# Kernel optimization log

Measured on AMD Instinct MI355X. Metric: run time of the kernel, lower is better.

Reference implementation:

```python
import jax, jax.numpy as jnp
import numpy as np

N_NODES = 8192
IN_F = 16384
OUT_F = 10
N_EDGES = 262144


def setup_inputs() -> dict:
    key = jax.random.key(0)
    ks = jax.random.split(key, 12)
    s = 0.02
    return {
        "x": jax.random.normal(ks[0], (N_NODES, IN_F), dtype=jnp.float32),
        "edge_index": jax.random.randint(ks[1], (2, N_EDGES), 0, N_NODES, dtype=jnp.int64),
        # lin1: in -> 4096, lin2: 4096 -> 2048 (torch Linear: y = x W^T + b)
        "lin1_w": jax.random.normal(ks[2], (4096, IN_F), dtype=jnp.float32) * s,
        "lin1_b": jnp.zeros((4096,), dtype=jnp.float32),
        "lin2_w": jax.random.normal(ks[3], (2048, 4096), dtype=jnp.float32) * s,
        "lin2_b": jnp.zeros((2048,), dtype=jnp.float32),
        # SAGEConv 1: 2048 -> 1024. lin_l (neighbor agg, with bias), lin_r (root, no bias)
        "s1_l_w": jax.random.normal(ks[4], (1024, 2048), dtype=jnp.float32) * s,
        "s1_l_b": jnp.zeros((1024,), dtype=jnp.float32),
        "s1_r_w": jax.random.normal(ks[5], (1024, 2048), dtype=jnp.float32) * s,
        # SAGEConv 2: 1024 -> OUT_F
        "s2_l_w": jax.random.normal(ks[6], (OUT_F, 1024), dtype=jnp.float32) * s,
        "s2_l_b": jnp.zeros((OUT_F,), dtype=jnp.float32),
        "s2_r_w": jax.random.normal(ks[7], (OUT_F, 1024), dtype=jnp.float32) * s,
    }


def reference(x, edge_index, lin1_w, lin1_b, lin2_w, lin2_b,
              s1_l_w, s1_l_b, s1_r_w, s2_l_w, s2_l_b, s2_r_w):
    n = x.shape[0]
    src, dst = edge_index[0], edge_index[1]
    # in-degree for mean aggregation; isolated nodes -> 0 aggregate (PyG behavior)
    deg = jax.ops.segment_sum(jnp.ones_like(dst, dtype=x.dtype), dst, num_segments=n)
    inv_deg = jnp.where(deg > 0, 1.0 / jnp.maximum(deg, 1.0), 0.0)[:, None]

    def sage(h, lw, lb, rw):
        # mean over incoming neighbor messages h[src] scattered to dst
        agg = jax.ops.segment_sum(h[src], dst, num_segments=n) * inv_deg
        return agg @ lw.T + lb + h @ rw.T

    h = jax.nn.relu(x @ lin1_w.T + lin1_b)
    h = jax.nn.relu(h @ lin2_w.T + lin2_b)
    # dropout layers act as identity in eval mode
    h = jax.nn.relu(sage(h, s1_l_w, s1_l_b, s1_r_w))
    h = jax.nn.relu(sage(h, s2_l_w, s2_l_b, s2_r_w))
    return jax.nn.softmax(h, axis=1)
```

## Files before the change

kernel.cpp:

```cpp
#include <hip/hip_runtime.h>


typedef short  short8   __attribute__((ext_vector_type(8)));
typedef float  floatx4  __attribute__((ext_vector_type(4)));
typedef unsigned short ushort8v __attribute__((ext_vector_type(8)));
typedef unsigned short ushort4v __attribute__((ext_vector_type(4)));
typedef unsigned short ushort;

__device__ __forceinline__ ushort f2bf(float f) {
  unsigned u = __float_as_uint(f);
  u += 0x7fffu + ((u >> 16) & 1u);
  return (ushort)(u >> 16);
}
__device__ __forceinline__ float bf2f(ushort h) {
  return __uint_as_float(((unsigned)h) << 16);
}

__device__ __forceinline__ void gload16(const void* g, void* l) {
  __builtin_amdgcn_global_load_lds(
      (const __attribute__((address_space(1))) void*)g,
      (__attribute__((address_space(3))) void*)l, 16, 0, 0);
}

__global__ __launch_bounds__(256) void cvt_f32_bf16(
    const float* __restrict__ in, ushort* __restrict__ out, long n8) {
  long i = (long)blockIdx.x * blockDim.x + threadIdx.x;
  const long stride = (long)gridDim.x * blockDim.x;
  for (; i < n8; i += stride) {
    const float4* p = (const float4*)(in + i * 8);
    float4 a = p[0], b = p[1];
    ushort8v o;
    o[0] = f2bf(a.x); o[1] = f2bf(a.y); o[2] = f2bf(a.z); o[3] = f2bf(a.w);
    o[4] = f2bf(b.x); o[5] = f2bf(b.y); o[6] = f2bf(b.z); o[7] = f2bf(b.w);
    *(ushort8v*)(out + i * 8) = o;
  }
}

__global__ void edge_count(const int* __restrict__ dst, int E, int* __restrict__ deg) {
  int e = blockIdx.x * 256 + threadIdx.x;
  if (e < E) atomicAdd(&deg[dst[e]], 1);
}

__global__ __launch_bounds__(256) void scan_k(
    const int* __restrict__ deg, int* __restrict__ offs, float* __restrict__ inv, int n) {
  __shared__ int part[256];
  const int t = threadIdx.x;
  int local[32];
  int s = 0;
  const int base = t * 32;
#pragma unroll
  for (int i = 0; i < 32; ++i) { local[i] = s; s += deg[base + i]; }
  part[t] = s;
  __syncthreads();
  for (int off = 1; off < 256; off <<= 1) {
    int v = (t >= off) ? part[t - off] : 0;
    __syncthreads();
    part[t] += v;
    __syncthreads();
  }
  const int prev = (t == 0) ? 0 : part[t - 1];
  if (t == 255) offs[n] = part[255];
#pragma unroll
  for (int i = 0; i < 32; ++i) {
    const int e = base + i;
    offs[e] = prev + local[i];
    const int d = deg[e];
    inv[e] = (d > 0) ? (1.0f / (float)d) : 0.0f;
  }
}

__global__ void edge_fill(const int* __restrict__ src, const int* __restrict__ dst, int E,
                          const int* __restrict__ offs, int* __restrict__ fill,
                          int* __restrict__ csr) {
  int e = blockIdx.x * 256 + threadIdx.x;
  if (e < E) {
    const int d = dst[e];
    const int p = offs[d] + atomicAdd(&fill[d], 1);
    csr[p] = src[e];
  }
}

template <int OUT_BF16, int RELU, int HAS_BIAS>
__global__ __launch_bounds__(512, 2) void gemm256(
    const ushort* __restrict__ A, const ushort* __restrict__ Bm,
    const float* __restrict__ bias, void* __restrict__ Cout,
    int M, int N, int K) {
  extern __shared__ char smem[];

  const int nbn = N >> 8;
  const int nbm8 = (M >> 8) >> 3;
  const int x = blockIdx.x & 7;
  const int j = blockIdx.x >> 3;
  const int bm = x * nbm8 + j / nbn;
  const int bn = j % nbn;

  const int t = threadIdx.x;
  const int w = t >> 6, lane = t & 63;
  const int wr = w >> 2, wc = w & 3;

  const int cswz = (t & 7) ^ ((t >> 3) & 7);
  const ushort* Ag = A  + (size_t)(bm * 256 + (t >> 3)) * K + cswz * 8;
  const ushort* Bg = Bm + (size_t)(bn * 256 + (t >> 3)) * K + cswz * 8;
  const int stOff = w * 1024;

  const int rA = wr * 128 + (lane & 15);
  const int rB = wc * 64 + (lane & 15);
  const int s0 = (((lane >> 4) ^ (lane & 7)) << 4);

  floatx4 acc[8][4] = {};
  const int NT = K >> 6;

  {
    char* la = smem + stOff;
    char* lb = la + 32768;
#pragma unroll
    for (int i = 0; i < 4; ++i) gload16(Ag + (size_t)(i * 64) * K, la + i * 8192);
#pragma unroll
    for (int i = 0; i < 4; ++i) gload16(Bg + (size_t)(i * 64) * K, lb + i * 8192);
  }
  __syncthreads();

  for (int kt = 0; kt < NT; ++kt) {
    const char* pa = smem + (kt & 1) * 65536 + rA * 128;
    const char* pb = smem + (kt & 1) * 65536 + 32768 + rB * 128;

    short8 a0[8], b0[4];
#pragma unroll
    for (int mi = 0; mi < 8; ++mi) a0[mi] = *(const short8*)(pa + mi * 2048 + s0);
#pragma unroll
    for (int ni = 0; ni < 4; ++ni) b0[ni] = *(const short8*)(pb + ni * 2048 + s0);

    if (kt + 1 < NT) {
      const int k0 = (kt + 1) << 6;
      char* la = smem + ((kt + 1) & 1) * 65536 + stOff;
      char* lb = la + 32768;
#pragma unroll
      for (int i = 0; i < 4; ++i) gload16(Ag + (size_t)(i * 64) * K + k0, la + i * 8192);
#pragma unroll
      for (int i = 0; i < 4; ++i) gload16(Bg + (size_t)(i * 64) * K + k0, lb + i * 8192);
    }

#pragma unroll
    for (int mi = 0; mi < 8; ++mi)
#pragma unroll
      for (int ni = 0; ni < 4; ++ni)
        acc[mi][ni] = __builtin_amdgcn_mfma_f32_16x16x32_bf16(a0[mi], b0[ni], acc[mi][ni], 0, 0, 0);

    short8 a1[8], b1[4];
#pragma unroll
    for (int mi = 0; mi < 8; ++mi) a1[mi] = *(const short8*)(pa + mi * 2048 + (s0 ^ 64));
#pragma unroll
    for (int ni = 0; ni < 4; ++ni) b1[ni] = *(const short8*)(pb + ni * 2048 + (s0 ^ 64));

#pragma unroll
    for (int mi = 0; mi < 8; ++mi)
#pragma unroll
      for (int ni = 0; ni < 4; ++ni)
        acc[mi][ni] = __builtin_amdgcn_mfma_f32_16x16x32_bf16(a1[mi], b1[ni], acc[mi][ni], 0, 0, 0);

    __syncthreads();
  }

  const int row0 = bm * 256 + wr * 128 + ((lane >> 4) << 2);
  const int col0 = bn * 256 + wc * 64 + (lane & 15);
#pragma unroll
  for (int ni = 0; ni < 4; ++ni) {
    const int col = col0 + ni * 16;
    const float bv = HAS_BIAS ? bias[col] : 0.0f;
#pragma unroll
    for (int mi = 0; mi < 8; ++mi) {
#pragma unroll
      for (int j2 = 0; j2 < 4; ++j2) {
        const int row = row0 + mi * 16 + j2;
        float v = acc[mi][ni][j2] + bv;
        if (RELU) v = fmaxf(v, 0.0f);
        if (OUT_BF16)
          ((ushort*)Cout)[(size_t)row * N + col] = f2bf(v);
        else
          ((float*)Cout)[(size_t)row * N + col] = v;
      }
    }
  }
}

__global__ __launch_bounds__(256) void sage1_agg(
    const ushort* __restrict__ hlr1, const int* __restrict__ offs,
    const int* __restrict__ csr, const float* __restrict__ inv,
    const float* __restrict__ lb, ushort* __restrict__ h3) {
  const int dn = blockIdx.x;
  const int f4 = threadIdx.x * 4;
  float ax = 0.f, ay = 0.f, az = 0.f, aw = 0.f;
  const int e0 = offs[dn], e1 = offs[dn + 1];
  for (int e = e0; e < e1; ++e) {
    const int s = csr[e];
    const ushort4v v = *(const ushort4v*)(hlr1 + (size_t)s * 2048 + f4);
    ax += bf2f(v[0]); ay += bf2f(v[1]); az += bf2f(v[2]); aw += bf2f(v[3]);
  }
  const float iv = inv[dn];
  const ushort4v hr = *(const ushort4v*)(hlr1 + (size_t)dn * 2048 + 1024 + f4);
  const float4 bb = *(const float4*)(lb + f4);
  ushort4v o;
  o[0] = f2bf(fmaxf(ax * iv + bb.x + bf2f(hr[0]), 0.0f));
  o[1] = f2bf(fmaxf(ay * iv + bb.y + bf2f(hr[1]), 0.0f));
  o[2] = f2bf(fmaxf(az * iv + bb.z + bf2f(hr[2]), 0.0f));
  o[3] = f2bf(fmaxf(aw * iv + bb.w + bf2f(hr[3]), 0.0f));
  *(ushort4v*)(h3 + (size_t)dn * 1024 + f4) = o;
}

__global__ __launch_bounds__(256) void sage2_mm(
    const ushort* __restrict__ h3, const float* __restrict__ wl,
    const float* __restrict__ wr, float* __restrict__ hl2, float* __restrict__ hr2) {
  __shared__ float wds[20480];
  const int t = threadIdx.x;
  for (int i = t; i < 2560; i += 256)
    *(float4*)&wds[i * 4] = *(const float4*)&wl[i * 4];
  for (int i = t; i < 2560; i += 256)
    *(float4*)&wds[10240 + i * 4] = *(const float4*)&wr[i * 4];
  __syncthreads();

  const int r = t >> 4, c = t & 15;
  const int row = blockIdx.x * 16 + r;

  float hv[64];
#pragma unroll
  for (int ii = 0; ii < 8; ++ii) {
    ushort8v p = *(const ushort8v*)(h3 + (size_t)row * 1024 + c * 64 + ii * 8);
#pragma unroll
    for (int k = 0; k < 8; ++k) hv[ii * 8 + k] = bf2f(p[k]);
  }

  float al[10] = {}, ar[10] = {};
#pragma unroll
  for (int j = 0; j < 10; ++j) {
    const int base = j * 1024 + c * 64;
#pragma unroll
    for (int ii = 0; ii < 16; ++ii) {
      const int f = (ii + c) & 15;
      const float4 lv = *(const float4*)&wds[base + f * 4];
      const float4 rv = *(const float4*)&wds[10240 + base + f * 4];
      const float h0 = hv[f * 4], h1 = hv[f * 4 + 1],
                  h2 = hv[f * 4 + 2], h3v = hv[f * 4 + 3];
      al[j] = fmaf(h0, lv.x, fmaf(h1, lv.y, fmaf(h2, lv.z, fmaf(h3v, lv.w, al[j]))));
      ar[j] = fmaf(h0, rv.x, fmaf(h1, rv.y, fmaf(h2, rv.z, fmaf(h3v, rv.w, ar[j]))));
    }
  }
#pragma unroll
  for (int j = 0; j < 10; ++j) {
#pragma unroll
    for (int off = 8; off > 0; off >>= 1) {
      al[j] += __shfl_down(al[j], off);
      ar[j] += __shfl_down(ar[j], off);
    }
  }
  if (c == 0) {
#pragma unroll
    for (int j = 0; j < 10; ++j) {
      hl2[(size_t)row * 10 + j] = al[j];
      hr2[(size_t)row * 10 + j] = ar[j];
    }
  }
}

__global__ __launch_bounds__(64) void sage2_final(
    const float* __restrict__ hl2, const float* __restrict__ hr2,
    const int* __restrict__ offs, const int* __restrict__ csr,
    const float* __restrict__ inv, const float* __restrict__ lb,
    float* __restrict__ out) {
  const int dn = blockIdx.x;
  const int l = threadIdx.x;
  float a[10] = {};
  const int e0 = offs[dn], e1 = offs[dn + 1];
  for (int e = e0 + l; e < e1; e += 64) {
    const int s = csr[e];
#pragma unroll
    for (int j = 0; j < 10; ++j) a[j] += hl2[(size_t)s * 10 + j];
  }
#pragma unroll
  for (int j = 0; j < 10; ++j)
#pragma unroll
    for (int off = 32; off > 0; off >>= 1) a[j] += __shfl_down(a[j], off);
  if (l == 0) {
    const float iv = inv[dn];
    float v[10];
    float m = -1e30f;
#pragma unroll
    for (int j = 0; j < 10; ++j) {
      v[j] = fmaxf(a[j] * iv + lb[j] + hr2[(size_t)dn * 10 + j], 0.0f);
      m = fmaxf(m, v[j]);
    }
    float ssum = 0.0f;
#pragma unroll
    for (int j = 0; j < 10; ++j) { v[j] = __expf(v[j] - m); ssum += v[j]; }
    const float r = 1.0f / ssum;
#pragma unroll
    for (int j = 0; j < 10; ++j) out[(size_t)dn * 10 + j] = v[j] * r;
  }
}

extern "C" void kernel_launch(void* const* d_in, const int* in_sizes, int n_in,
                              void* d_out, int out_size, void* d_ws, size_t ws_size,
                              hipStream_t stream) {
  const float* x    = (const float*)d_in[0];
  const int*   ei   = (const int*)d_in[1];
  const float* w1   = (const float*)d_in[2];
  const float* b1   = (const float*)d_in[3];
  const float* w2   = (const float*)d_in[4];
  const float* b2   = (const float*)d_in[5];
  const float* s1lw = (const float*)d_in[6];
  const float* s1lb = (const float*)d_in[7];
  const float* s1rw = (const float*)d_in[8];
  const float* s2lw = (const float*)d_in[9];
  const float* s2lb = (const float*)d_in[10];
  const float* s2rw = (const float*)d_in[11];
  float* out = (float*)d_out;
  char* ws = (char*)d_ws;

  const int E = in_sizes[1] / 2;
  const int Nn = 8192;

  hipFuncSetAttribute((const void*)&gemm256<1, 1, 1>,
                      hipFuncAttributeMaxDynamicSharedMemorySize, 131072);
  hipFuncSetAttribute((const void*)&gemm256<1, 0, 0>,
                      hipFuncAttributeMaxDynamicSharedMemorySize, 131072);

  ushort* xb  = (ushort*)(ws + 0L);
  ushort* w1b = (ushort*)(ws + 268435456L);
  ushort* h1  = (ushort*)(ws + 402653184L);
  ushort* w2b = (ushort*)(ws + 469762048L);
  ushort* h2  = (ushort*)(ws + 486539264L);
  ushort* ws1 = (ushort*)(ws + 520093696L);
  char* csrb = ws + 528482304L;
  int*   deg  = (int*)(csrb);
  int*   fill = (int*)(csrb + 32768);
  int*   offs = (int*)(csrb + 65536);
  float* inv  = (float*)(csrb + 98816);
  int*   csr  = (int*)(csrb + 131584);
  ushort* hlr1 = (ushort*)(ws + 0L);
  ushort* h3   = (ushort*)(ws + 67108864L);
  float*  hl2  = (float*)(ws + 83886080L);
  float*  hr2  = (float*)(ws + 84213760L);

  const int* esrc = ei;
  const int* edst = ei + E;

  hipMemsetAsync(deg, 0, 65536, stream);

  cvt_f32_bf16<<<4096, 256, 0, stream>>>(x, xb, 16777216L);
  cvt_f32_bf16<<<2048, 256, 0, stream>>>(w1, w1b, 8388608L);
  cvt_f32_bf16<<<1024, 256, 0, stream>>>(w2, w2b, 1048576L);
  cvt_f32_bf16<<<256, 256, 0, stream>>>(s1lw, ws1, 262144L);
  cvt_f32_bf16<<<256, 256, 0, stream>>>(s1rw, ws1 + 2097152L, 262144L);

  edge_count<<<(E + 255) / 256, 256, 0, stream>>>(edst, E, deg);
  scan_k<<<1, 256, 0, stream>>>(deg, offs, inv, Nn);
  edge_fill<<<(E + 255) / 256, 256, 0, stream>>>(esrc, edst, E, offs, fill, csr);

  gemm256<1, 1, 1><<<512, 512, 131072, stream>>>(xb, w1b, b1, h1, 8192, 4096, 16384);
  gemm256<1, 1, 1><<<256, 512, 131072, stream>>>(h1, w2b, b2, h2, 8192, 2048, 4096);
  gemm256<1, 0, 0><<<256, 512, 131072, stream>>>(h2, ws1, nullptr, hlr1, 8192, 2048, 2048);

  sage1_agg<<<8192, 256, 0, stream>>>(hlr1, offs, csr, inv, s1lb, h3);
  sage2_mm<<<512, 256, 0, stream>>>(h3, s2lw, s2rw, hl2, hr2);
  sage2_final<<<8192, 64, 0, stream>>>(hl2, hr2, offs, csr, inv, s2lb, out);
}
```

Before: 1.673 ms.

## Restructure GEMM main loop into fine-grained phases with interleaved async loads

Replaces the simple double-buffered k-loop with an 8-phase schedule per two k-tiles. Each phase reads a slice of A fragments, issues a portion of the next tile's global-to-LDS loads, waits with explicit vmcnt counts, and raises wave priority around the MFMA bursts. The goal is to hide global load latency and LDS reads behind MFMA work instead of stalling at a full __syncthreads each tile. It relies on hand-tuned waitcnt values and per-phase barriers, assumes NT is even, and issues dummy loads past the last tile.

```diff
diff --git a/kernel.cpp b/kernel.cpp
--- a/kernel.cpp
+++ b/kernel.cpp
@@ -109,57 +109,83 @@
 
   floatx4 acc[8][4] = {};
   const int NT = K >> 6;
-
-  {
-    char* la = smem + stOff;
-    char* lb = la + 32768;
-#pragma unroll
-    for (int i = 0; i < 4; ++i) gload16(Ag + (size_t)(i * 64) * K, la + i * 8192);
-#pragma unroll
-    for (int i = 0; i < 4; ++i) gload16(Bg + (size_t)(i * 64) * K, lb + i * 8192);
-  }
-  __syncthreads();
-
-  for (int kt = 0; kt < NT; ++kt) {
-    const char* pa = smem + (kt & 1) * 65536 + rA * 128;
-    const char* pb = smem + (kt & 1) * 65536 + 32768 + rB * 128;
-
-    short8 a0[8], b0[4];
-#pragma unroll
-    for (int mi = 0; mi < 8; ++mi) a0[mi] = *(const short8*)(pa + mi * 2048 + s0);
-#pragma unroll
-    for (int ni = 0; ni < 4; ++ni) b0[ni] = *(const short8*)(pb + ni * 2048 + s0);
-
-    if (kt + 1 < NT) {
-      const int k0 = (kt + 1) << 6;
-      char* la = smem + ((kt + 1) & 1) * 65536 + stOff;
-      char* lb = la + 32768;
-#pragma unroll
-      for (int i = 0; i < 4; ++i) gload16(Ag + (size_t)(i * 64) * K + k0, la + i * 8192);
-#pragma unroll
-      for (int i = 0; i < 4; ++i) gload16(Bg + (size_t)(i * 64) * K + k0, lb + i * 8192);
-    }
-
-#pragma unroll
-    for (int mi = 0; mi < 8; ++mi)
-#pragma unroll
-      for (int ni = 0; ni < 4; ++ni)
-        acc[mi][ni] = __builtin_amdgcn_mfma_f32_16x16x32_bf16(a0[mi], b0[ni], acc[mi][ni], 0, 0, 0);
-
-    short8 a1[8], b1[4];
-#pragma unroll
-    for (int mi = 0; mi < 8; ++mi) a1[mi] = *(const short8*)(pa + mi * 2048 + (s0 ^ 64));
-#pragma unroll
-    for (int ni = 0; ni < 4; ++ni) b1[ni] = *(const short8*)(pb + ni * 2048 + (s0 ^ 64));
-
-#pragma unroll
-    for (int mi = 0; mi < 8; ++mi)
-#pragma unroll
-      for (int ni = 0; ni < 4; ++ni)
-        acc[mi][ni] = __builtin_amdgcn_mfma_f32_16x16x32_bf16(a1[mi], b1[ni], acc[mi][ni], 0, 0, 0);
-
-    __syncthreads();
-  }
+  const int NIT = NT >> 1;
+
+#define STGA(BUF, KT, H)                                                      \
+  {                                                                           \
+    const int k0_ = (((KT) < NT) ? (KT) : 0) << 6;                            \
+    char* la_ = smem + (BUF) * 65536 + stOff;                                 \
+    gload16(Ag + (size_t)(((H) * 2) * 64) * K + k0_, la_ + ((H) * 2) * 8192); \
+    gload16(Ag + (size_t)(((H) * 2 + 1) * 64) * K + k0_,                      \
+            la_ + ((H) * 2 + 1) * 8192);                                      \
+  }
+#define STGB(BUF, KT, H)                                                      \
+  {                                                                           \
+    const int k0_ = (((KT) < NT) ? (KT) : 0) << 6;                            \
+    char* lb_ = smem + (BUF) * 65536 + 32768 + stOff;                         \
+    gload16(Bg + (size_t)(((H) * 2) * 64) * K + k0_, lb_ + ((H) * 2) * 8192); \
+    gload16(Bg + (size_t)(((H) * 2 + 1) * 64) * K + k0_,                      \
+            lb_ + ((H) * 2 + 1) * 8192);                                      \
+  }
+
+#define PH(BUF, Q, READB, DOWAIT, ...)                                        \
+  {                                                                           \
+    const char* pa_ = smem + (BUF) * 65536 + rA * 128;                        \
+    short8 a00 = *(const short8*)(pa_ + (2 * (Q)) * 2048 + s0);               \
+    short8 a01 = *(const short8*)(pa_ + (2 * (Q)) * 2048 + (s0 ^ 64));        \
+    short8 a10 = *(const short8*)(pa_ + (2 * (Q) + 1) * 2048 + s0);           \
+    short8 a11 = *(const short8*)(pa_ + (2 * (Q) + 1) * 2048 + (s0 ^ 64));    \
+    if (READB) {                                                              \
+      const char* pb_ = smem + (BUF) * 65536 + 32768 + rB * 128;              \
+      _Pragma("unroll") for (int ni = 0; ni < 4; ++ni) {                      \
+        bfv0[ni] = *(const short8*)(pb_ + ni * 2048 + s0);                    \
+        bfv1[ni] = *(const short8*)(pb_ + ni * 2048 + (s0 ^ 64));             \
+      }                                                                       \
+    }                                                                         \
+    __VA_ARGS__;                                                              \
+    if (DOWAIT) asm volatile("s_waitcnt vmcnt(4)" ::: "memory");              \
+    __builtin_amdgcn_s_barrier();                                             \
+    __builtin_amdgcn_s_setprio(1);                                            \
+    _Pragma("unroll") for (int ni = 0; ni < 4; ++ni) {                        \
+      acc[2 * (Q)][ni] = __builtin_amdgcn_mfma_f32_16x16x32_bf16(             \
+          a00, bfv0[ni], acc[2 * (Q)][ni], 0, 0, 0);                          \
+      acc[2 * (Q) + 1][ni] = __builtin_amdgcn_mfma_f32_16x16x32_bf16(         \
+          a10, bfv0[ni], acc[2 * (Q) + 1][ni], 0, 0, 0);                      \
+    }                                                                         \
+    _Pragma("unroll") for (int ni = 0; ni < 4; ++ni) {                        \
+      acc[2 * (Q)][ni] = __builtin_amdgcn_mfma_f32_16x16x32_bf16(             \
+          a01, bfv1[ni], acc[2 * (Q)][ni], 0, 0, 0);                          \
+      acc[2 * (Q) + 1][ni] = __builtin_amdgcn_mfma_f32_16x16x32_bf16(         \
+          a11, bfv1[ni], acc[2 * (Q) + 1][ni], 0, 0, 0);                      \
+    }                                                                         \
+    __builtin_amdgcn_s_setprio(0);                                            \
+    asm volatile("" ::: "memory");                                            \
+  }
+
+  STGA(0, 0, 0); STGA(0, 0, 1);
+  STGB(0, 0, 0); STGB(0, 0, 1);
+  STGB(1, 1, 0); STGB(1, 1, 1);
+  asm volatile("s_waitcnt vmcnt(4)" ::: "memory");
+  __builtin_amdgcn_s_barrier();
+  asm volatile("" ::: "memory");
+
+  for (int it = 0; it < NIT; ++it) {
+    const int t1 = 2 * it + 1, t2 = 2 * it + 2, t3 = 2 * it + 3;
+    short8 bfv0[4], bfv1[4];
+    PH(0, 0, 1, 0, STGA(1, t1, 0); STGA(1, t1, 1));
+    PH(0, 1, 0, 0, STGB(0, t2, 0));
+    PH(0, 2, 0, 0, STGB(0, t2, 1));
+    PH(0, 3, 0, 1, );
+    PH(1, 0, 1, 0, STGA(0, t2, 0));
+    PH(1, 1, 0, 0, STGA(0, t2, 1));
+    PH(1, 2, 0, 0, STGB(1, t3, 0));
+    PH(1, 3, 0, 1, STGB(1, t3, 1));
+  }
+  asm volatile("s_waitcnt vmcnt(0)" ::: "memory");
+
+#undef STGA
+#undef STGB
+#undef PH
 
   const int row0 = bm * 256 + wr * 128 + ((lane >> 4) << 2);
   const int col0 = bn * 256 + wc * 64 + (lane & 15);
```

Measured after the change: 1.365 ms. -18.4%, faster.
